# Performance work log

Hardware: AMD Instinct MI355X
Metric: run time of the kernel (lower is better)

Reference implementation:

```python
import jax, jax.numpy as jnp
import numpy as np

B, S, C, M, L = 32, 8192, 64, 16, 4  # batch, seq, n_enc, n_modes, n_layers


def setup_inputs() -> dict:
    key = jax.random.key(0)
    ks = jax.random.split(key, 12)
    scale = 1.0 / (C * M)
    return {
        "input_tensor": jax.random.normal(ks[0], (B, S, 1), dtype=jnp.float32),
        "enc_w": jax.random.normal(ks[1], (C, 1), dtype=jnp.float32) * 0.1,
        "enc_b": jax.random.normal(ks[2], (C,), dtype=jnp.float32) * 0.1,
        "R_re": jax.random.normal(ks[3], (L, C, C, M), dtype=jnp.float32) * scale,
        "R_im": jax.random.normal(ks[4], (L, C, C, M), dtype=jnp.float32) * scale,
        "Wl_w": jax.random.normal(ks[5], (L, C, C), dtype=jnp.float32) * 0.1,
        "Wl_b": jax.random.normal(ks[6], (L, C), dtype=jnp.float32) * 0.1,
        "d1_w": jax.random.normal(ks[7], (C, C), dtype=jnp.float32) * 0.1,
        "d1_b": jax.random.normal(ks[8], (C,), dtype=jnp.float32) * 0.1,
        "d2_w": jax.random.normal(ks[9], (1, C), dtype=jnp.float32) * 0.1,
        "d2_b": jax.random.normal(ks[10], (1,), dtype=jnp.float32) * 0.1,
    }


def reference(input_tensor, enc_w, enc_b, R_re, R_im, Wl_w, Wl_b, d1_w, d1_b, d2_w, d2_b):
    # encoder: Conv1d(1, C, k=1) == per-position dense over channel dim
    h = jnp.einsum('bsi,ci->bsc', input_tensor, enc_w) + enc_b  # [B,S,C]
    n_freq = S // 2 + 1
    for l in range(L):
        x_cs = jnp.swapaxes(h, 1, 2)                 # [B,C,S]
        x_ft = jnp.fft.rfft(x_cs, axis=-1)           # [B,C,n_freq] complex
        Rl = R_re[l] + 1j * R_im[l]                  # [C,C,M]
        y = jnp.einsum('bim,iom->bom', x_ft[:, :, :M], Rl)  # [B,C,M]
        y_full = jnp.concatenate(
            [y, jnp.zeros((B, C, n_freq - M), dtype=y.dtype)], axis=-1)
        spat = jnp.fft.irfft(y_full, n=S, axis=-1)   # [B,C,S] float32
        wout = jnp.einsum('oi,bis->bos', Wl_w[l], x_cs) + Wl_b[l][None, :, None]
        h = jax.nn.gelu(jnp.swapaxes(spat + wout, 1, 2), approximate=False)
    z = jax.nn.gelu(jnp.einsum('bsc,oc->bso', h, d1_w) + d1_b, approximate=False)
    out = jnp.einsum('bso,po->bsp', z, d2_w) + d2_b  # [B,S,1]
    return out
```

## Files before the change

kernel.cpp:

```cpp
#include <hip/hip_runtime.h>
#include <math.h>

#define NB 32
#define NS 8192
#define NC 64
#define NM 16
#define NL 4
#define NM2 32
#define TPOS 128
#define NT (NS/TPOS)
#define PAD 65
#define APAD 68
#define GPAD 132

typedef float f16v  __attribute__((ext_vector_type(16)));
typedef float f4v   __attribute__((ext_vector_type(4)));
typedef short bf16x8 __attribute__((ext_vector_type(8)));
typedef short bf16x4 __attribute__((ext_vector_type(4)));

#define MFMA16(a,b,c) __builtin_amdgcn_mfma_f32_16x16x32_bf16(a,b,c,0,0,0)

static __device__ __forceinline__ unsigned short f2bf(float x) {
    unsigned u = __float_as_uint(x);
    u += 0x7FFFu + ((u >> 16) & 1u);
    return (unsigned short)(u >> 16);
}
static __device__ __forceinline__ float bf2f(unsigned short b) {
    return __uint_as_float(((unsigned)b) << 16);
}
static __device__ __forceinline__ bf16x8 ld8l(const unsigned short* p) {
    bf16x4 a = *(const bf16x4*)p;
    bf16x4 b = *(const bf16x4*)(p + 4);
    return __builtin_shufflevector(a, b, 0, 1, 2, 3, 4, 5, 6, 7);
}
static __device__ __forceinline__ float gelu_exact(float v) {
    return 0.5f * v * (1.0f + erff(v * 0.7071067811865475f));
}

__global__ void k_table(float* __restrict__ T,
                        unsigned short* __restrict__ Thi,
                        unsigned short* __restrict__ Tlo,
                        unsigned short* __restrict__ TThi,
                        unsigned short* __restrict__ TTlo) {
    int s = blockIdx.x * 256 + threadIdx.x;
    if (s >= NS) return;
    const float w = 6.283185307179586f / (float)NS;
    #pragma unroll
    for (int m = 0; m < NM; ++m) {
        int idx = (m * s) & (NS - 1);
        float sv, cv;
        sincosf(w * (float)idx, &sv, &cv);
        T[(size_t)s*NM2 + 2*m]   = cv;
        T[(size_t)s*NM2 + 2*m+1] = sv;
        unsigned short ch = f2bf(cv), cl = f2bf(cv - bf2f(f2bf(cv)));
        unsigned short sh = f2bf(sv), sl = f2bf(sv - bf2f(f2bf(sv)));
        Thi[(size_t)s*NM2 + 2*m]   = ch;  Tlo[(size_t)s*NM2 + 2*m]   = cl;
        Thi[(size_t)s*NM2 + 2*m+1] = sh;  Tlo[(size_t)s*NM2 + 2*m+1] = sl;
        TThi[(size_t)(2*m)*NS + s]   = ch;  TTlo[(size_t)(2*m)*NS + s]   = cl;
        TThi[(size_t)(2*m+1)*NS + s] = sh;  TTlo[(size_t)(2*m+1)*NS + s] = sl;
    }
}

__global__ void k_prep(const float* __restrict__ Ww, const float* __restrict__ d1w,
                       unsigned short* __restrict__ Wbhi,
                       unsigned short* __restrict__ Wblo,
                       float* __restrict__ d1t) {
    int idx = blockIdx.x * 256 + threadIdx.x;
    if (idx < NL*NC*NC) {
        float v = Ww[idx];
        unsigned short hi = f2bf(v);
        Wbhi[idx] = hi;
        Wblo[idx] = f2bf(v - bf2f(hi));
    } else if (idx < NL*NC*NC + NC*NC) {
        int r = idx - NL*NC*NC;
        int i = r / NC, o = r % NC;
        d1t[r] = d1w[(size_t)o*NC + i];
    }
}

static __device__ __forceinline__ void dft_phase(
        const float* __restrict__ hs, const float* __restrict__ T,
        float* __restrict__ partial, int b, int tile, int s0, int t) {
    int c  = t & 63;
    int kg = __builtin_amdgcn_readfirstlane(t >> 6);
    f4v acc = {0.f, 0.f, 0.f, 0.f};
    const float* trow = T + (size_t)s0 * NM2 + kg * 4;
    #pragma unroll 4
    for (int ss = 0; ss < TPOS; ++ss) {
        float hv = hs[ss * PAD + c];
        f4v tv = *(const f4v*)(trow + (size_t)ss * NM2);
        acc += hv * tv;
    }
    float* pout = partial + (((size_t)b*NT + tile)*NC + c)*NM2 + kg*4;
    *(f4v*)pout = acc;
}

__global__ void __launch_bounds__(512) k_enc(const float* __restrict__ x,
                                             const float* __restrict__ ew,
                                             const float* __restrict__ eb,
                                             const float* __restrict__ T,
                                             float* __restrict__ h,
                                             float* __restrict__ partial) {
    __shared__ float hs[TPOS * PAD];
    int tile = blockIdx.x, b = blockIdx.y;
    int t = threadIdx.x;
    int og = __builtin_amdgcn_readfirstlane(t >> 7);
    int p  = t & 127;
    int s0 = tile * TPOS;

    float xv = x[(size_t)b*NS + s0 + p];
    f16v ew16 = *(const f16v*)(ew + og*16);
    f16v eb16 = *(const f16v*)(eb + og*16);
    f16v hv = xv * ew16 + eb16;

    *(f16v*)(h + ((size_t)b*NS + s0 + p)*NC + og*16) = hv;

    #pragma unroll
    for (int j = 0; j < 16; ++j) hs[p*PAD + og*16 + j] = hv[j];
    __syncthreads();

    dft_phase(hs, T, partial, b, tile, s0, t);
}

__global__ void __launch_bounds__(256) k_mix(const float* __restrict__ partial,
                                             const float* __restrict__ Rre,
                                             const float* __restrict__ Rim,
                                             unsigned short* __restrict__ ysbThi,
                                             unsigned short* __restrict__ ysbTlo,
                                             int l) {
    __shared__ float xf[NC * 8];
    int b = blockIdx.x, jg = blockIdx.y, t = threadIdx.x;
    #pragma unroll
    for (int e = 0; e < 2; ++e) {
        int idx = t + 256*e;
        int c = idx >> 3, kk = idx & 7;
        const float* pp = partial + (size_t)b*NT*NC*NM2 + (size_t)c*NM2 + 8*jg + kk;
        float s = 0.f;
        #pragma unroll 8
        for (int tile = 0; tile < NT; ++tile)
            s += pp[(size_t)tile * NC * NM2];
        xf[idx] = s;
    }
    __syncthreads();
    {
        int o = t >> 2, mq = t & 3;
        int m = 4*jg + mq;
        float yre = 0.f, yim = 0.f;
        #pragma unroll 8
        for (int i = 0; i < NC; ++i) {
            float xr = xf[i*8 + 2*mq];
            float xs = xf[i*8 + 2*mq + 1];
            size_t ridx = (((size_t)l*NC + i)*NC + o)*NM + m;
            float rr = Rre[ridx], ri = Rim[ridx];
            yre = fmaf(xr, rr, yre); yre = fmaf(xs, ri, yre);
            yim = fmaf(xr, ri, yim); yim = fmaf(-xs, rr, yim);
        }
        float v0, v1;
        if (m == 0) { v0 = yre * (1.0f/NS); v1 = 0.f; }
        else        { v0 = yre * (2.0f/NS); v1 = -yim * (2.0f/NS); }
        size_t yb = ((size_t)b*NC + o)*NM2;
        unsigned short h0 = f2bf(v0);
        ysbThi[yb + 2*m]   = h0;  ysbTlo[yb + 2*m]   = f2bf(v0 - bf2f(h0));
        unsigned short h1 = f2bf(v1);
        ysbThi[yb + 2*m+1] = h1;  ysbTlo[yb + 2*m+1] = f2bf(v1 - bf2f(h1));
    }
}

template<bool LAST>
__global__ void __launch_bounds__(512) k_spec(float* __restrict__ h,
                                              const unsigned short* __restrict__ Thi,
                                              const unsigned short* __restrict__ Tlo,
                                              const unsigned short* __restrict__ TThi,
                                              const unsigned short* __restrict__ TTlo,
                                              const unsigned short* __restrict__ ysbThi,
                                              const unsigned short* __restrict__ ysbTlo,
                                              const unsigned short* __restrict__ Wbhi,
                                              const unsigned short* __restrict__ Wblo,
                                              const float* __restrict__ Wlb,
                                              const float* __restrict__ d1t,
                                              const float* __restrict__ d1b,
                                              const float* __restrict__ d2w,
                                              const float* __restrict__ d2b,
                                              float* __restrict__ partial,
                                              float* __restrict__ outp,
                                              int l) {
    __shared__ __align__(16) unsigned short uLDS[2 * TPOS * APAD];
    unsigned short* hsAhi = uLDS;
    unsigned short* hsAlo = uLDS + TPOS * APAD;

    int tile = blockIdx.x, b = blockIdx.y;
    int t = threadIdx.x;
    int lane = t & 63, w = t >> 6;
    int lm = lane & 15, g = lane >> 4;
    int s0 = tile * TPOS;

    const float4* hblk = (const float4*)(h + ((size_t)b*NS + s0)*NC);
    #pragma unroll
    for (int j = 0; j < 4; ++j) {
        float4 v = hblk[t + 512*j];
        int idx = t + 512*j;
        int pos = idx >> 4, q4 = (idx & 15) * 4;
        float vv[4] = {v.x, v.y, v.z, v.w};
        bf16x4 hi4, lo4;
        #pragma unroll
        for (int e = 0; e < 4; ++e) {
            unsigned short hh = f2bf(vv[e]);
            hi4[e] = (short)hh;
            lo4[e] = (short)f2bf(vv[e] - bf2f(hh));
        }
        *(bf16x4*)(&hsAhi[pos*APAD + q4]) = hi4;
        *(bf16x4*)(&hsAlo[pos*APAD + q4]) = lo4;
    }
    __syncthreads();

    bf16x8 aHi[2], aLo[2];
    #pragma unroll
    for (int k2 = 0; k2 < 2; ++k2) {
        int eo = (w*16 + lm)*APAD + k2*32 + 8*g;
        aHi[k2] = ld8l(&hsAhi[eo]);
        aLo[k2] = ld8l(&hsAlo[eo]);
    }
    bf16x8 tHi = *(const bf16x8*)(Thi + (size_t)(s0 + w*16 + lm)*NM2 + 8*g);
    bf16x8 tLo = *(const bf16x8*)(Tlo + (size_t)(s0 + w*16 + lm)*NM2 + 8*g);

    f4v acc[4];
    #pragma unroll
    for (int N = 0; N < 4; ++N) {
        float bv = Wlb[(size_t)l*NC + N*16 + lm];
        acc[N] = (f4v){bv, bv, bv, bv};
    }

    #pragma unroll
    for (int N = 0; N < 4; ++N) {
        size_t yo = ((size_t)b*NC + N*16 + lm)*NM2 + 8*g;
        bf16x8 yHi = *(const bf16x8*)(ysbThi + yo);
        bf16x8 yLo = *(const bf16x8*)(ysbTlo + yo);
        acc[N] = MFMA16(tHi, yHi, acc[N]);
        acc[N] = MFMA16(tHi, yLo, acc[N]);
        acc[N] = MFMA16(tLo, yHi, acc[N]);
    }

    #pragma unroll
    for (int k2 = 0; k2 < 2; ++k2) {
        #pragma unroll
        for (int N = 0; N < 4; ++N) {
            size_t wo = ((size_t)l*NC + N*16 + lm)*NC + k2*32 + 8*g;
            bf16x8 wHi = *(const bf16x8*)(Wbhi + wo);
            bf16x8 wLo = *(const bf16x8*)(Wblo + wo);
            acc[N] = MFMA16(aHi[k2], wHi, acc[N]);
            acc[N] = MFMA16(aHi[k2], wLo, acc[N]);
            acc[N] = MFMA16(aLo[k2], wHi, acc[N]);
        }
    }

    f4v gv[4];
    #pragma unroll
    for (int N = 0; N < 4; ++N)
        #pragma unroll
        for (int r = 0; r < 4; ++r)
            gv[N][r] = gelu_exact(acc[N][r]);

    if (!LAST) {
        #pragma unroll
        for (int N = 0; N < 4; ++N)
            #pragma unroll
            for (int r = 0; r < 4; ++r)
                h[((size_t)b*NS + s0 + w*16 + g*4 + r)*NC + N*16 + lm] = gv[N][r];
    }

    __syncthreads();

    if (!LAST) {
        unsigned short* gThi = uLDS;
        unsigned short* gTlo = uLDS + NC * GPAD;
        #pragma unroll
        for (int N = 0; N < 4; ++N) {
            int c = N*16 + lm;
            #pragma unroll
            for (int r = 0; r < 4; ++r) {
                int pos = w*16 + g*4 + r;
                float v = gv[N][r];
                unsigned short hh = f2bf(v);
                gThi[c*GPAD + pos] = hh;
                gTlo[c*GPAD + pos] = f2bf(v - bf2f(hh));
            }
        }
        __syncthreads();

        int Mblk = w & 3, Nblk = w >> 2;
        f4v pacc = {0.f, 0.f, 0.f, 0.f};
        #pragma unroll
        for (int ks = 0; ks < 4; ++ks) {
            int eo = (Mblk*16 + lm)*GPAD + ks*32 + 8*g;
            bf16x8 gHi = ld8l(&gThi[eo]);
            bf16x8 gLo = ld8l(&gTlo[eo]);
            size_t to = (size_t)(Nblk*16 + lm)*NS + s0 + ks*32 + 8*g;
            bf16x8 tbHi = *(const bf16x8*)(TThi + to);
            bf16x8 tbLo = *(const bf16x8*)(TTlo + to);
            pacc = MFMA16(gHi, tbHi, pacc);
            pacc = MFMA16(gHi, tbLo, pacc);
            pacc = MFMA16(gLo, tbHi, pacc);
        }
        float* pout = partial + ((size_t)b*NT + tile)*NC*NM2;
        #pragma unroll
        for (int r = 0; r < 4; ++r) {
            int c = Mblk*16 + g*4 + r;
            pout[(size_t)c*NM2 + Nblk*16 + lm] = pacc[r];
        }
    } else {
        float* hsf = (float*)uLDS;
        #pragma unroll
        for (int N = 0; N < 4; ++N)
            #pragma unroll
            for (int r = 0; r < 4; ++r)
                hsf[(w*16 + g*4 + r)*PAD + N*16 + lm] = gv[N][r];
        __syncthreads();

        int og2 = __builtin_amdgcn_readfirstlane(t >> 7);
        int p2  = t & 127;
        f16v a = *(const f16v*)(d1b + og2*16);
        const float* hr = hsf + p2*PAD;
        #pragma unroll 8
        for (int i = 0; i < NC; ++i) {
            float hv = hr[i];
            f16v wv = *(const f16v*)(d1t + (size_t)i*NC + og2*16);
            a += hv * wv;
        }
        float res = 0.f;
        #pragma unroll
        for (int j = 0; j < 16; ++j)
            res = fmaf(gelu_exact(a[j]), d2w[og2*16 + j], res);
        __syncthreads();
        hsf[og2*TPOS + p2] = res;
        __syncthreads();
        if (t < TPOS) {
            outp[(size_t)b*NS + s0 + t] = d2b[0] + hsf[t] + hsf[TPOS + t]
                                        + hsf[2*TPOS + t] + hsf[3*TPOS + t];
        }
    }
}

extern "C" void kernel_launch(void* const* d_in, const int* in_sizes, int n_in,
                              void* d_out, int out_size, void* d_ws, size_t ws_size,
                              hipStream_t stream) {
    const float* input = (const float*)d_in[0];
    const float* enc_w = (const float*)d_in[1];
    const float* enc_b = (const float*)d_in[2];
    const float* R_re  = (const float*)d_in[3];
    const float* R_im  = (const float*)d_in[4];
    const float* Wl_w  = (const float*)d_in[5];
    const float* Wl_b  = (const float*)d_in[6];
    const float* d1_w  = (const float*)d_in[7];
    const float* d1_b  = (const float*)d_in[8];
    const float* d2_w  = (const float*)d_in[9];
    const float* d2_b  = (const float*)d_in[10];
    float* out = (float*)d_out;

    float* ws  = (float*)d_ws;
    float* h   = ws;
    float* T   = h   + (size_t)NB*NS*NC;
    float* par = T   + (size_t)NS*NM2;
    float* d1t = par + (size_t)NB*NT*NC*NM2;
    unsigned short* Thi    = (unsigned short*)(d1t + NC*NC);
    unsigned short* Tlo    = Thi    + (size_t)NS*NM2;
    unsigned short* TThi   = Tlo    + (size_t)NS*NM2;
    unsigned short* TTlo   = TThi   + (size_t)NM2*NS;
    unsigned short* ysbThi = TTlo   + (size_t)NM2*NS;
    unsigned short* ysbTlo = ysbThi + (size_t)NB*NC*NM2;
    unsigned short* Wbhi   = ysbTlo + (size_t)NB*NC*NM2;
    unsigned short* Wblo   = Wbhi   + (size_t)NL*NC*NC;

    hipLaunchKernelGGL(k_table, dim3(NS/256), dim3(256), 0, stream,
                       T, Thi, Tlo, TThi, TTlo);
    hipLaunchKernelGGL(k_prep, dim3((NL*NC*NC + NC*NC + 255)/256), dim3(256), 0,
                       stream, Wl_w, d1_w, Wbhi, Wblo, d1t);
    hipLaunchKernelGGL(k_enc, dim3(NT, NB), dim3(512), 0, stream,
                       input, enc_w, enc_b, T, h, par);
    for (int l = 0; l < NL; ++l) {
        hipLaunchKernelGGL(k_mix, dim3(NB, 4), dim3(256), 0, stream,
                           par, R_re, R_im, ysbThi, ysbTlo, l);
        if (l < NL - 1) {
            hipLaunchKernelGGL((k_spec<false>), dim3(NT, NB), dim3(512), 0, stream,
                               h, Thi, Tlo, TThi, TTlo, ysbThi, ysbTlo,
                               Wbhi, Wblo, Wl_b, d1t, d1_b, d2_w, d2_b,
                               par, out, l);
        } else {
            hipLaunchKernelGGL((k_spec<true>), dim3(NT, NB), dim3(512), 0, stream,
                               h, Thi, Tlo, TThi, TTlo, ysbThi, ysbTlo,
                               Wbhi, Wblo, Wl_b, d1t, d1_b, d2_w, d2_b,
                               par, out, l);
        }
    }
}
```

Baseline: 360.7 us.

## Drop encoder h buffer, use linear DFT of input, pack bf16 hi/lo activations

The first layer's DFT is now computed from the raw input with one small per-batch DFT kernel, relying on the encoder being affine (X = ew*DFT(x) + eb*S at mode 0). The encoder is recomputed inside the first spectral kernel, so the full-size encoder activation is never written or read. Intermediate activations are stored as packed bf16 hi/lo pairs instead of fp32 stores followed by reconversion, and the partial DFT layout is transposed for coalesced writes. The decoder in the last layer moves to split-bf16 MFMA with a shuffle reduction. The cost is extra code complexity and the precision of the 3-term bf16 split in the decoder.

Result: slower. 368.7 us (+2.2%).

```diff
diff --git a/kernel.cpp b/kernel.cpp
--- a/kernel.cpp
+++ b/kernel.cpp
@@ -9,7 +9,6 @@
 #define NM2 32
 #define TPOS 128
 #define NT (NS/TPOS)
-#define PAD 65
 #define APAD 68
 #define GPAD 132
 
@@ -64,7 +63,8 @@
 __global__ void k_prep(const float* __restrict__ Ww, const float* __restrict__ d1w,
                        unsigned short* __restrict__ Wbhi,
                        unsigned short* __restrict__ Wblo,
-                       float* __restrict__ d1t) {
+                       unsigned short* __restrict__ d1hi,
+                       unsigned short* __restrict__ d1lo) {
     int idx = blockIdx.x * 256 + threadIdx.x;
     if (idx < NL*NC*NC) {
         float v = Ww[idx];
@@ -73,73 +73,62 @@
         Wblo[idx] = f2bf(v - bf2f(hi));
     } else if (idx < NL*NC*NC + NC*NC) {
         int r = idx - NL*NC*NC;
-        int i = r / NC, o = r % NC;
-        d1t[r] = d1w[(size_t)o*NC + i];
-    }
-}
-
-static __device__ __forceinline__ void dft_phase(
-        const float* __restrict__ hs, const float* __restrict__ T,
-        float* __restrict__ partial, int b, int tile, int s0, int t) {
-    int c  = t & 63;
-    int kg = __builtin_amdgcn_readfirstlane(t >> 6);
-    f4v acc = {0.f, 0.f, 0.f, 0.f};
-    const float* trow = T + (size_t)s0 * NM2 + kg * 4;
+        float v = d1w[r];
+        unsigned short hi = f2bf(v);
+        d1hi[r] = hi;
+        d1lo[r] = f2bf(v - bf2f(hi));
+    }
+}
+
+__global__ void __launch_bounds__(512) k_xdft(const float* __restrict__ x,
+                                              const float* __restrict__ T,
+                                              float* __restrict__ X) {
+    __shared__ float red[16 * NM2];
+    int b = blockIdx.x, t = threadIdx.x;
+    int k = t & 31, sg = t >> 5;
+    float acc = 0.f;
     #pragma unroll 4
-    for (int ss = 0; ss < TPOS; ++ss) {
-        float hv = hs[ss * PAD + c];
-        f4v tv = *(const f4v*)(trow + (size_t)ss * NM2);
-        acc += hv * tv;
-    }
-    float* pout = partial + (((size_t)b*NT + tile)*NC + c)*NM2 + kg*4;
-    *(f4v*)pout = acc;
-}
-
-__global__ void __launch_bounds__(512) k_enc(const float* __restrict__ x,
-                                             const float* __restrict__ ew,
-                                             const float* __restrict__ eb,
-                                             const float* __restrict__ T,
-                                             float* __restrict__ h,
-                                             float* __restrict__ partial) {
-    __shared__ float hs[TPOS * PAD];
-    int tile = blockIdx.x, b = blockIdx.y;
-    int t = threadIdx.x;
-    int og = __builtin_amdgcn_readfirstlane(t >> 7);
-    int p  = t & 127;
-    int s0 = tile * TPOS;
-
-    float xv = x[(size_t)b*NS + s0 + p];
-    f16v ew16 = *(const f16v*)(ew + og*16);
-    f16v eb16 = *(const f16v*)(eb + og*16);
-    f16v hv = xv * ew16 + eb16;
-
-    *(f16v*)(h + ((size_t)b*NS + s0 + p)*NC + og*16) = hv;
-
-    #pragma unroll
-    for (int j = 0; j < 16; ++j) hs[p*PAD + og*16 + j] = hv[j];
+    for (int it = 0; it < NS/16; ++it) {
+        int s = sg * (NS/16) + it;
+        acc = fmaf(x[(size_t)b*NS + s], T[(size_t)s*NM2 + k], acc);
+    }
+    red[sg*NM2 + k] = acc;
     __syncthreads();
-
-    dft_phase(hs, T, partial, b, tile, s0, t);
+    if (t < NM2) {
+        float s = 0.f;
+        #pragma unroll
+        for (int q = 0; q < 16; ++q) s += red[q*NM2 + t];
+        X[(size_t)b*NM2 + t] = s;
+    }
 }
 
 __global__ void __launch_bounds__(256) k_mix(const float* __restrict__ partial,
                                              const float* __restrict__ Rre,
                                              const float* __restrict__ Rim,
+                                             const float* __restrict__ X,
+                                             const float* __restrict__ ew,
+                                             const float* __restrict__ eb,
                                              unsigned short* __restrict__ ysbThi,
                                              unsigned short* __restrict__ ysbTlo,
                                              int l) {
-    __shared__ float xf[NC * 8];
+    __shared__ float xf[8 * NC];
     int b = blockIdx.x, jg = blockIdx.y, t = threadIdx.x;
     #pragma unroll
     for (int e = 0; e < 2; ++e) {
         int idx = t + 256*e;
-        int c = idx >> 3, kk = idx & 7;
-        const float* pp = partial + (size_t)b*NT*NC*NM2 + (size_t)c*NM2 + 8*jg + kk;
-        float s = 0.f;
-        #pragma unroll 8
-        for (int tile = 0; tile < NT; ++tile)
-            s += pp[(size_t)tile * NC * NM2];
-        xf[idx] = s;
+        int kk = idx >> 6, c = idx & 63;
+        int k = 8*jg + kk;
+        float s;
+        if (l == 0) {
+            s = ew[c] * X[(size_t)b*NM2 + k] + (k == 0 ? eb[c] * (float)NS : 0.f);
+        } else {
+            const float* pp = partial + (size_t)b*NT*NC*NM2 + (size_t)k*NC + c;
+            s = 0.f;
+            #pragma unroll 8
+            for (int tile = 0; tile < NT; ++tile)
+                s += pp[(size_t)tile * NC * NM2];
+        }
+        xf[kk*NC + c] = s;
     }
     __syncthreads();
     {
@@ -148,8 +137,8 @@
         float yre = 0.f, yim = 0.f;
         #pragma unroll 8
         for (int i = 0; i < NC; ++i) {
-            float xr = xf[i*8 + 2*mq];
-            float xs = xf[i*8 + 2*mq + 1];
+            float xr = xf[(2*mq)*NC + i];
+            float xs = xf[(2*mq+1)*NC + i];
             size_t ridx = (((size_t)l*NC + i)*NC + o)*NM + m;
             float rr = Rre[ridx], ri = Rim[ridx];
             yre = fmaf(xr, rr, yre); yre = fmaf(xs, ri, yre);
@@ -166,8 +155,9 @@
     }
 }
 
-template<bool LAST>
-__global__ void __launch_bounds__(512) k_spec(float* __restrict__ h,
+template<bool FIRST, bool LAST>
+__global__ void __launch_bounds__(512) k_spec(const float* __restrict__ x,
+                                              unsigned* __restrict__ hpk,
                                               const unsigned short* __restrict__ Thi,
                                               const unsigned short* __restrict__ Tlo,
                                               const unsigned short* __restrict__ TThi,
@@ -177,10 +167,13 @@
                                               const unsigned short* __restrict__ Wbhi,
                                               const unsigned short* __restrict__ Wblo,
                                               const float* __restrict__ Wlb,
-                                              const float* __restrict__ d1t,
+                                              const unsigned short* __restrict__ d1hi,
+                                              const unsigned short* __restrict__ d1lo,
                                               const float* __restrict__ d1b,
                                               const float* __restrict__ d2w,
                                               const float* __restrict__ d2b,
+                                              const float* __restrict__ ew,
+                                              const float* __restrict__ eb,
                                               float* __restrict__ partial,
                                               float* __restrict__ outp,
                                               int l) {
@@ -194,22 +187,42 @@
     int lm = lane & 15, g = lane >> 4;
     int s0 = tile * TPOS;
 
-    const float4* hblk = (const float4*)(h + ((size_t)b*NS + s0)*NC);
-    #pragma unroll
-    for (int j = 0; j < 4; ++j) {
-        float4 v = hblk[t + 512*j];
-        int idx = t + 512*j;
-        int pos = idx >> 4, q4 = (idx & 15) * 4;
-        float vv[4] = {v.x, v.y, v.z, v.w};
-        bf16x4 hi4, lo4;
-        #pragma unroll
-        for (int e = 0; e < 4; ++e) {
-            unsigned short hh = f2bf(vv[e]);
-            hi4[e] = (short)hh;
-            lo4[e] = (short)f2bf(vv[e] - bf2f(hh));
-        }
-        *(bf16x4*)(&hsAhi[pos*APAD + q4]) = hi4;
-        *(bf16x4*)(&hsAlo[pos*APAD + q4]) = lo4;
+    if (FIRST) {
+        #pragma unroll
+        for (int j = 0; j < 4; ++j) {
+            int idx = t + 512*j;
+            int pos = idx >> 4, q4 = (idx & 15) * 4;
+            float xv = x[(size_t)b*NS + s0 + pos];
+            f4v w4 = *(const f4v*)(ew + q4);
+            f4v b4 = *(const f4v*)(eb + q4);
+            bf16x4 hi4, lo4;
+            #pragma unroll
+            for (int e = 0; e < 4; ++e) {
+                float v = fmaf(xv, w4[e], b4[e]);
+                unsigned short hh = f2bf(v);
+                hi4[e] = (short)hh;
+                lo4[e] = (short)f2bf(v - bf2f(hh));
+            }
+            *(bf16x4*)(&hsAhi[pos*APAD + q4]) = hi4;
+            *(bf16x4*)(&hsAlo[pos*APAD + q4]) = lo4;
+        }
+    } else {
+        const uint4* hblk = (const uint4*)(hpk + ((size_t)b*NS + s0)*NC);
+        #pragma unroll
+        for (int j = 0; j < 4; ++j) {
+            uint4 v = hblk[t + 512*j];
+            int idx = t + 512*j;
+            int pos = idx >> 4, q4 = (idx & 15) * 4;
+            unsigned vv[4] = {v.x, v.y, v.z, v.w};
+            bf16x4 hi4, lo4;
+            #pragma unroll
+            for (int e = 0; e < 4; ++e) {
+                hi4[e] = (short)(vv[e] >> 16);
+                lo4[e] = (short)(vv[e] & 0xFFFFu);
+            }
+            *(bf16x4*)(&hsAhi[pos*APAD + q4]) = hi4;
+            *(bf16x4*)(&hsAlo[pos*APAD + q4]) = lo4;
+        }
     }
     __syncthreads();
 
@@ -260,14 +273,6 @@
         for (int r = 0; r < 4; ++r)
             gv[N][r] = gelu_exact(acc[N][r]);
 
-    if (!LAST) {
-        #pragma unroll
-        for (int N = 0; N < 4; ++N)
-            #pragma unroll
-            for (int r = 0; r < 4; ++r)
-                h[((size_t)b*NS + s0 + w*16 + g*4 + r)*NC + N*16 + lm] = gv[N][r];
-    }
-
     __syncthreads();
 
     if (!LAST) {
@@ -281,8 +286,11 @@
                 int pos = w*16 + g*4 + r;
                 float v = gv[N][r];
                 unsigned short hh = f2bf(v);
+                unsigned short ll = f2bf(v - bf2f(hh));
                 gThi[c*GPAD + pos] = hh;
-                gTlo[c*GPAD + pos] = f2bf(v - bf2f(hh));
+                gTlo[c*GPAD + pos] = ll;
+                hpk[((size_t)b*NS + s0 + pos)*NC + c] =
+                    ((unsigned)hh << 16) | (unsigned)ll;
             }
         }
         __syncthreads();
@@ -302,41 +310,64 @@
             pacc = MFMA16(gLo, tbHi, pacc);
         }
         float* pout = partial + ((size_t)b*NT + tile)*NC*NM2;
+        int k = Nblk*16 + lm;
+        *(f4v*)(pout + (size_t)k*NC + Mblk*16 + g*4) = pacc;
+    } else {
+        #pragma unroll
+        for (int N = 0; N < 4; ++N) {
+            int c = N*16 + lm;
+            #pragma unroll
+            for (int r = 0; r < 4; ++r) {
+                int pos = w*16 + g*4 + r;
+                float v = gv[N][r];
+                unsigned short hh = f2bf(v);
+                hsAhi[pos*APAD + c] = hh;
+                hsAlo[pos*APAD + c] = f2bf(v - bf2f(hh));
+            }
+        }
+        __syncthreads();
+
+        bf16x8 gH[2], gL[2];
+        #pragma unroll
+        for (int k2 = 0; k2 < 2; ++k2) {
+            int eo = (w*16 + lm)*APAD + k2*32 + 8*g;
+            gH[k2] = ld8l(&hsAhi[eo]);
+            gL[k2] = ld8l(&hsAlo[eo]);
+        }
+        f4v a2[4];
+        #pragma unroll
+        for (int N = 0; N < 4; ++N) {
+            float bv = d1b[N*16 + lm];
+            a2[N] = (f4v){bv, bv, bv, bv};
+        }
+        #pragma unroll
+        for (int k2 = 0; k2 < 2; ++k2) {
+            #pragma unroll
+            for (int N = 0; N < 4; ++N) {
+                size_t wo = ((size_t)(N*16 + lm))*NC + k2*32 + 8*g;
+                bf16x8 wHi = *(const bf16x8*)(d1hi + wo);
+                bf16x8 wLo = *(const bf16x8*)(d1lo + wo);
+                a2[N] = MFMA16(gH[k2], wHi, a2[N]);
+                a2[N] = MFMA16(gH[k2], wLo, a2[N]);
+                a2[N] = MFMA16(gL[k2], wHi, a2[N]);
+            }
+        }
+        float tr[4];
         #pragma unroll
         for (int r = 0; r < 4; ++r) {
-            int c = Mblk*16 + g*4 + r;
-            pout[(size_t)c*NM2 + Nblk*16 + lm] = pacc[r];
-        }
-    } else {
-        float* hsf = (float*)uLDS;
-        #pragma unroll
-        for (int N = 0; N < 4; ++N)
-            #pragma unroll
-            for (int r = 0; r < 4; ++r)
-                hsf[(w*16 + g*4 + r)*PAD + N*16 + lm] = gv[N][r];
-        __syncthreads();
-
-        int og2 = __builtin_amdgcn_readfirstlane(t >> 7);
-        int p2  = t & 127;
-        f16v a = *(const f16v*)(d1b + og2*16);
-        const float* hr = hsf + p2*PAD;
-        #pragma unroll 8
-        for (int i = 0; i < NC; ++i) {
-            float hv = hr[i];
-            f16v wv = *(const f16v*)(d1t + (size_t)i*NC + og2*16);
-            a += hv * wv;
-        }
-        float res = 0.f;
-        #pragma unroll
-        for (int j = 0; j < 16; ++j)
-            res = fmaf(gelu_exact(a[j]), d2w[og2*16 + j], res);
-        __syncthreads();
-        hsf[og2*TPOS + p2] = res;
-        __syncthreads();
-        if (t < TPOS) {
-            outp[(size_t)b*NS + s0 + t] = d2b[0] + hsf[t] + hsf[TPOS + t]
-                                        + hsf[2*TPOS + t] + hsf[3*TPOS + t];
-        }
+            float s = 0.f;
+            #pragma unroll
+            for (int N = 0; N < 4; ++N)
+                s = fmaf(gelu_exact(a2[N][r]), d2w[N*16 + lm], s);
+            s += __shfl_xor(s, 1);
+            s += __shfl_xor(s, 2);
+            s += __shfl_xor(s, 4);
+            s += __shfl_xor(s, 8);
+            tr[r] = s;
+        }
+        float val = (lm == 1) ? tr[1] : (lm == 2) ? tr[2] : (lm == 3) ? tr[3] : tr[0];
+        if (lm < 4)
+            outp[(size_t)b*NS + s0 + w*16 + g*4 + lm] = d2b[0] + val;
     }
 }
 
@@ -357,11 +388,11 @@
     float* out = (float*)d_out;
 
     float* ws  = (float*)d_ws;
-    float* h   = ws;
-    float* T   = h   + (size_t)NB*NS*NC;
+    unsigned* hpk = (unsigned*)ws;
+    float* T   = ws  + (size_t)NB*NS*NC;
     float* par = T   + (size_t)NS*NM2;
-    float* d1t = par + (size_t)NB*NT*NC*NM2;
-    unsigned short* Thi    = (unsigned short*)(d1t + NC*NC);
+    float* X   = par + (size_t)NB*NT*NC*NM2;
+    unsigned short* Thi    = (unsigned short*)(X + (size_t)NB*NM2);
     unsigned short* Tlo    = Thi    + (size_t)NS*NM2;
     unsigned short* TThi   = Tlo    + (size_t)NS*NM2;
     unsigned short* TTlo   = TThi   + (size_t)NM2*NS;
@@ -369,25 +400,35 @@
     unsigned short* ysbTlo = ysbThi + (size_t)NB*NC*NM2;
     unsigned short* Wbhi   = ysbTlo + (size_t)NB*NC*NM2;
     unsigned short* Wblo   = Wbhi   + (size_t)NL*NC*NC;
+    unsigned short* d1hi   = Wblo   + (size_t)NL*NC*NC;
+    unsigned short* d1lo   = d1hi   + (size_t)NC*NC;
 
     hipLaunchKernelGGL(k_table, dim3(NS/256), dim3(256), 0, stream,
                        T, Thi, Tlo, TThi, TTlo);
     hipLaunchKernelGGL(k_prep, dim3((NL*NC*NC + NC*NC + 255)/256), dim3(256), 0,
-                       stream, Wl_w, d1_w, Wbhi, Wblo, d1t);
-    hipLaunchKernelGGL(k_enc, dim3(NT, NB), dim3(512), 0, stream,
-                       input, enc_w, enc_b, T, h, par);
+                       stream, Wl_w, d1_w, Wbhi, Wblo, d1hi, d1lo);
+    hipLaunchKernelGGL(k_xdft, dim3(NB), dim3(512), 0, stream, input, T, X);
     for (int l = 0; l < NL; ++l) {
         hipLaunchKernelGGL(k_mix, dim3(NB, 4), dim3(256), 0, stream,
-                           par, R_re, R_im, ysbThi, ysbTlo, l);
-        if (l < NL - 1) {
-            hipLaunchKernelGGL((k_spec<false>), dim3(NT, NB), dim3(512), 0, stream,
-                               h, Thi, Tlo, TThi, TTlo, ysbThi, ysbTlo,
-                               Wbhi, Wblo, Wl_b, d1t, d1_b, d2_w, d2_b,
+                           par, R_re, R_im, X, enc_w, enc_b,
+                           ysbThi, ysbTlo, l);
+        if (l == 0) {
+            hipLaunchKernelGGL((k_spec<true, false>), dim3(NT, NB), dim3(512), 0,
+                               stream, input, hpk, Thi, Tlo, TThi, TTlo,
+                               ysbThi, ysbTlo, Wbhi, Wblo, Wl_b,
+                               d1hi, d1lo, d1_b, d2_w, d2_b, enc_w, enc_b,
+                               par, out, l);
+        } else if (l < NL - 1) {
+            hipLaunchKernelGGL((k_spec<false, false>), dim3(NT, NB), dim3(512), 0,
+                               stream, input, hpk, Thi, Tlo, TThi, TTlo,
+                               ysbThi, ysbTlo, Wbhi, Wblo, Wl_b,
+                               d1hi, d1lo, d1_b, d2_w, d2_b, enc_w, enc_b,
                                par, out, l);
         } else {
-            hipLaunchKernelGGL((k_spec<true>), dim3(NT, NB), dim3(512), 0, stream,
-                               h, Thi, Tlo, TThi, TTlo, ysbThi, ysbTlo,
-                               Wbhi, Wblo, Wl_b, d1t, d1_b, d2_w, d2_b,
+            hipLaunchKernelGGL((k_spec<false, true>), dim3(NT, NB), dim3(512), 0,
+                               stream, input, hpk, Thi, Tlo, TThi, TTlo,
+                               ysbThi, ysbTlo, Wbhi, Wblo, Wl_b,
+                               d1hi, d1lo, d1_b, d2_w, d2_b, enc_w, enc_b,
                                par, out, l);
         }
     }
```
